# Kernel tuning notes

Hardware: AMD Instinct MI355X
Metric: run time of the kernel (lower is better)

Reference implementation:

```python
import jax, jax.numpy as jnp
import numpy as np

D = 1024
H = 16
HD = D // H  # 64

def setup_inputs() -> dict:
    key = jax.random.key(0)
    ks = jax.random.split(key, 7)
    B, S = 2, 2048
    x = jax.random.normal(ks[0], (B, S, D), dtype=jnp.float32)
    M = jax.random.randint(ks[1], (B, S, S), 0, 2, dtype=jnp.int32)
    s = 1.0 / np.sqrt(D)
    W_q = jax.random.normal(ks[2], (D, D), dtype=jnp.float32) * s
    W_k = jax.random.normal(ks[3], (D, D), dtype=jnp.float32) * s
    W_v = jax.random.normal(ks[4], (D, D), dtype=jnp.float32) * s
    W_o = jax.random.normal(ks[5], (D, D), dtype=jnp.float32) * s
    b_o = jax.random.normal(ks[6], (D,), dtype=jnp.float32) * 0.01
    return {"x": x, "M": M, "W_q": W_q, "W_k": W_k, "W_v": W_v, "W_o": W_o, "b_o": b_o}

def reference(x, M, W_q, W_k, W_v, W_o, b_o):
    B, S, _ = x.shape
    scale = HD ** -0.5
    # project and split heads: [B, H, S, HD]
    def heads(W):
        return (x @ W.T).reshape(B, S, H, HD).transpose(0, 2, 1, 3)
    Q, K, V = heads(W_q), heads(W_k), heads(W_v)
    scores = jnp.einsum('bhqd,bhkd->bhqk', Q, K) * scale
    mask = (M[:, None, :, :] == 0)  # broadcast over heads
    scores = jnp.where(mask, jnp.float32(-1e9), scores)
    A = jax.nn.softmax(scores, axis=-1)
    out = jnp.einsum('bhqk,bhkd->bhqd', A, V)
    out = out.transpose(0, 2, 1, 3).reshape(B, S, D)
    return out @ W_o.T + b_o
```

## Files before the change

### kernel.cpp

```cpp
#include <hip/hip_runtime.h>
#include <hip/hip_bf16.h>

typedef unsigned short u16;
typedef unsigned int u32;
typedef unsigned long long u64;
typedef _Float16 f16;
typedef __attribute__((__ext_vector_type__(4))) _Float16 f16x4;
typedef __attribute__((__ext_vector_type__(8))) short bf16x8;
typedef __attribute__((__ext_vector_type__(4))) float f32x4;
typedef __attribute__((__ext_vector_type__(16))) float f32x16;

__device__ __forceinline__ u16 f2bf(float f) {
    u32 u = __float_as_uint(f);
    return (u16)((u + 0x7fffu + ((u >> 16) & 1u)) >> 16);
}

__device__ __forceinline__ u32 pk2(float e, float o) {
    return (__float_as_uint(e) >> 16) | (__float_as_uint(o) & 0xFFFF0000u);
}

__global__ __launch_bounds__(256) void prep_kernel(
    const float4* __restrict__ x,  const float4* __restrict__ wq,
    const float4* __restrict__ wk, const float4* __restrict__ wv,
    const float4* __restrict__ wo,
    u16* __restrict__ xb, u16* __restrict__ wqb, u16* __restrict__ wkb,
    u16* __restrict__ wvb, u16* __restrict__ wob,
    const int* __restrict__ M, u64* __restrict__ Mb2)
{
    if (blockIdx.x < 8192) {
        int gid = blockIdx.x * 256 + threadIdx.x;
        const float4* src; u16* dst; int off;
        if (gid < 1048576) { src = x; dst = xb; off = gid; }
        else {
            int g = gid - 1048576;
            int sel = g >> 18;
            off = g & 262143;
            src = sel == 0 ? wq : sel == 1 ? wk : sel == 2 ? wv : wo;
            dst = sel == 0 ? wqb : sel == 1 ? wkb : sel == 2 ? wvb : wob;
        }
        float4 f = src[off];
        ushort4 o;
        o.x = f2bf(f.x); o.y = f2bf(f.y); o.z = f2bf(f.z); o.w = f2bf(f.w);
        ((ushort4*)dst)[off] = o;
    } else {
        int wg   = (blockIdx.x - 8192) * 4 + (threadIdx.x >> 6);
        int lane = threadIdx.x & 63;
        int w = wg & 31;
        int q = (wg >> 5) & 2047;
        int b = wg >> 16;
        size_t base = ((size_t)(b * 2048 + q)) * 2048 + w * 64 + lane;
        u64 bits = __ballot(M[base] != 0);
        if (lane == 0) Mb2[(size_t)(b * 32 + w) * 2048 + q] = bits;
    }
}

template<int MODE, int BN>
__global__ __launch_bounds__(256) void gemm_k(
    const u16* __restrict__ Ag, const u16* __restrict__ Bg,
    u16* __restrict__ Cq, u16* __restrict__ Kfr, u16* __restrict__ Vfr,
    float* __restrict__ Cf, const float* __restrict__ bias)
{
    constexpr int Kd = 1024;
    constexpr int NB = BN / 32;
    __shared__ u16 SM[8192 + BN * 64];
    u16* As0 = SM;
    u16* As1 = SM + 4096;
    u16* Bs0 = SM + 8192;
    u16* Bs1 = SM + 8192 + BN * 32;
    const int tid  = threadIdx.x;
    const int wave = tid >> 6, lane = tid & 63;
    const int quad = lane >> 4, l16 = lane & 15;
    const int n0 = blockIdx.x * BN;
    const int m0 = blockIdx.y * 128;

    const int wm = (wave & 1) * 64, wn = (wave >> 1) * (BN / 2);
    f32x4 acc[4][NB];
    #pragma unroll
    for (int i = 0; i < 4; i++)
        #pragma unroll
        for (int j = 0; j < NB; j++)
            acc[i][j] = (f32x4){0.f, 0.f, 0.f, 0.f};

    const int sr = lane >> 2;
    const int sk = (lane & 3) * 8;
    const int ca0 = wave * 2, ca1 = ca0 + 1;
    const u16* gA0 = Ag + (size_t)(m0 + ca0 * 16 + sr) * Kd + sk;
    const u16* gA1 = Ag + (size_t)(m0 + ca1 * 16 + sr) * Kd + sk;
    const int cb0 = (BN == 128) ? wave * 2 : wave;
    const u16* gB0 = Bg + (size_t)(n0 + cb0 * 16 + sr) * Kd + sk;
    const u16* gB1 = (BN == 128) ? Bg + (size_t)(n0 + (cb0 + 1) * 16 + sr) * Kd + sk : nullptr;

    #define GLL16(gp, lp) __builtin_amdgcn_global_load_lds( \
        (const __attribute__((address_space(1))) void*)(gp), \
        (__attribute__((address_space(3))) void*)(lp), 16, 0, 0)

    for (int k0 = 0; k0 < Kd; k0 += 64) {
        __syncthreads();
        GLL16(gA0 + k0, As0 + ca0 * 512);
        GLL16(gA1 + k0, As0 + ca1 * 512);
        GLL16(gB0 + k0, Bs0 + cb0 * 512);
        if (BN == 128) GLL16(gB1 + k0, Bs0 + (cb0 + 1) * 512);
        GLL16(gA0 + k0 + 32, As1 + ca0 * 512);
        GLL16(gA1 + k0 + 32, As1 + ca1 * 512);
        GLL16(gB0 + k0 + 32, Bs1 + cb0 * 512);
        if (BN == 128) GLL16(gB1 + k0 + 32, Bs1 + (cb0 + 1) * 512);
        __syncthreads();

        #pragma unroll
        for (int kk = 0; kk < 2; kk++) {
            const u16* Ah = kk ? As1 : As0;
            const u16* Bh = kk ? Bs1 : Bs0;
            bf16x8 af[4], bfr[NB];
            #pragma unroll
            for (int mb = 0; mb < 4; mb++)
                af[mb] = *(const bf16x8*)&Ah[(wm + mb * 16 + l16) * 32 + quad * 8];
            #pragma unroll
            for (int nb = 0; nb < NB; nb++)
                bfr[nb] = *(const bf16x8*)&Bh[(wn + nb * 16 + l16) * 32 + quad * 8];
            #pragma unroll
            for (int mb = 0; mb < 4; mb++)
                #pragma unroll
                for (int nb = 0; nb < NB; nb++)
                    acc[mb][nb] = __builtin_amdgcn_mfma_f32_16x16x32_bf16(
                        af[mb], bfr[nb], acc[mb][nb], 0, 0, 0);
        }
    }
    #undef GLL16

    if (MODE == 1) {
        #pragma unroll
        for (int mb = 0; mb < 4; mb++)
            #pragma unroll
            for (int nb = 0; nb < NB; nb++) {
                const int row = m0 + wm + mb * 16 + quad * 4;
                const int col = n0 + wn + nb * 16 + l16;
                #pragma unroll
                for (int r = 0; r < 4; r++)
                    Cf[(size_t)(row + r) * 1024 + col] = acc[mb][nb][r] + bias[col];
            }
        return;
    }

    const int region = n0 >> 10;
    if (region == 0) {
        #pragma unroll
        for (int mb = 0; mb < 4; mb++)
            #pragma unroll
            for (int nb = 0; nb < NB; nb++) {
                const int row = m0 + wm + mb * 16 + quad * 4;
                const int ccol = (n0 & 1023) + wn + nb * 16 + l16;
                #pragma unroll
                for (int r = 0; r < 4; r++)
                    Cq[(size_t)(row + r) * 1024 + ccol] =
                        f2bf(acc[mb][nb][r] * 0.18033688011112042f);
            }
        return;
    }

    const int bb = m0 >> 11;
    const int kt_base = (m0 & 2047) >> 6;
    const int head_base = (n0 & 1023) >> 6;
    u16* dst = (region == 1) ? Kfr : Vfr;
    #pragma unroll
    for (int pass = 0; pass < 2; pass++) {
        __syncthreads();
        #pragma unroll
        for (int mb = 0; mb < 4; mb++) {
            const int rowb = wm + mb * 16 + quad * 4;
            if ((rowb >> 6) != pass) continue;
            #pragma unroll
            for (int nb = 0; nb < NB; nb++) {
                const int ccol = wn + nb * 16 + l16;
                const int h2 = ccol >> 6, dd = ccol & 63;
                if (region == 1) {
                    const int t = dd >> 4, hik = (dd >> 3) & 1, j = dd & 7;
                    #pragma unroll
                    for (int r = 0; r < 4; r++) {
                        const int km = (rowb + r) & 63;
                        const int f = (km >> 5) * 4 + t;
                        const int lanek = hik * 32 + (km & 31);
                        SM[((h2 * 8 + f) * 64 + lanek) * 8 + j] = f2bf(acc[mb][nb][r]);
                    }
                } else {
                    const int kinb = rowb & 63;
                    const int t = kinb >> 4, hiv = (kinb >> 3) & 1, jb = kinb & 7;
                    const int f = (dd >> 5) * 4 + t;
                    const int lanev = hiv * 32 + (dd & 31);
                    ushort4 pk;
                    pk.x = f2bf(acc[mb][nb][0]); pk.y = f2bf(acc[mb][nb][1]);
                    pk.z = f2bf(acc[mb][nb][2]); pk.w = f2bf(acc[mb][nb][3]);
                    *(ushort4*)&SM[((h2 * 8 + f) * 64 + lanev) * 8 + jb] = pk;
                }
            }
        }
        __syncthreads();
        const int h2g = tid >> 7;
        const int inner = (tid & 127) * 32;
        const size_t gbase =
            ((size_t)(bb * 16 + head_base + h2g) * 32 + kt_base + pass) * 4096;
        #pragma unroll
        for (int c = 0; c < 4; c++)
            *(bf16x8*)&dst[gbase + inner + c * 8] =
                *(const bf16x8*)&SM[h2g * 4096 + inner + c * 8];
    }
}

__global__ __launch_bounds__(256) void attn_kernel(
    const u16* __restrict__ Qg, const u16* __restrict__ Kfr, const u16* __restrict__ Vfr,
    const u64* __restrict__ Mb2, f16* __restrict__ Opart, float* __restrict__ Lpart)
{
    const int qt = blockIdx.x >> 2;
    const int kh = blockIdx.x & 3;
    const int h  = blockIdx.y;
    const int b  = blockIdx.z;
    const int tid = threadIdx.x, wave = tid >> 6, lane = tid & 63;
    const int l31 = lane & 31, hi = lane >> 5;

    const int qrow0 = qt * 128 + wave * 32;
    const int bh    = b * 16 + h;

    bf16x8 qf[4];
    {
        const u16* qp = Qg + ((size_t)b * 2048 + qrow0 + l31) * 1024 + h * 64 + hi * 8;
        #pragma unroll
        for (int t = 0; t < 4; t++) qf[t] = *(const bf16x8*)(qp + t * 16);
    }

    const u16* kfp = Kfr + (size_t)bh * 131072 + lane * 8;
    const u16* vfp = Vfr + (size_t)bh * 131072 + lane * 8;

    f32x16 oacc0, oacc1;
    #pragma unroll
    for (int i = 0; i < 16; i++) { oacc0[i] = 0.f; oacc1[i] = 0.f; }
    float lsum = 0.f;

    const int kt0 = kh * 8;
    #pragma unroll 1
    for (int kt = kt0; kt < kt0 + 8; kt++) {
        const u64 mwv = Mb2[(size_t)(b * 32 + kt) * 2048 + qrow0 + l31];
        const u32 mlo = ((u32)mwv) >> (hi * 4);
        const u32 mhi = ((u32)(mwv >> 32)) >> (hi * 4);
        const size_t fb = (size_t)(kt * 8) * 512;

        #pragma unroll
        for (int ph = 0; ph < 2; ph++) {
            bf16x8 kf[4], vf[4];
            #pragma unroll
            for (int t = 0; t < 4; t++)
                kf[t] = *(const bf16x8*)(kfp + fb + (size_t)(ph * 4 + t) * 512);
            vf[0] = *(const bf16x8*)(vfp + fb + (size_t)(2 * ph) * 512);
            vf[1] = *(const bf16x8*)(vfp + fb + (size_t)(2 * ph + 1) * 512);
            vf[2] = *(const bf16x8*)(vfp + fb + (size_t)(4 + 2 * ph) * 512);
            vf[3] = *(const bf16x8*)(vfp + fb + (size_t)(4 + 2 * ph + 1) * 512);

            f32x16 s;
            #pragma unroll
            for (int i = 0; i < 16; i++) s[i] = 0.f;
            #pragma unroll
            for (int t = 0; t < 4; t++)
                s = __builtin_amdgcn_mfma_f32_32x32x16_bf16(kf[t], qf[t], s, 0, 0, 0);

            const u32 mm = ph ? mhi : mlo;
            #pragma unroll
            for (int reg = 0; reg < 16; reg++) {
                const int kb2 = (reg & 3) + 8 * (reg >> 2);
                float a = __builtin_amdgcn_exp2f(s[reg]);
                a = ((mm >> kb2) & 1u) ? a : 0.0f;
                s[reg] = a; lsum += a;
            }

            bf16x8 pb[2];
            #pragma unroll
            for (int fl = 0; fl < 2; fl++) {
                const int rb = 8 * fl;
                u32 a0 = pk2(s[rb], s[rb + 1]),     a1 = pk2(s[rb + 2], s[rb + 3]);
                u32 a2 = pk2(s[rb + 4], s[rb + 5]), a3 = pk2(s[rb + 6], s[rb + 7]);
                const u32 r0 = __shfl_xor(a0, 32);
                const u32 r1 = __shfl_xor(a1, 32);
                const u32 r2 = __shfl_xor(a2, 32);
                const u32 r3 = __shfl_xor(a3, 32);
                union { u32 u[4]; bf16x8 v; } fu;
                fu.u[0] = hi ? r2 : a0;
                fu.u[1] = hi ? r3 : a1;
                fu.u[2] = hi ? a2 : r0;
                fu.u[3] = hi ? a3 : r1;
                pb[fl] = fu.v;
            }

            oacc0 = __builtin_amdgcn_mfma_f32_32x32x16_bf16(vf[0], pb[0], oacc0, 0, 0, 0);
            oacc0 = __builtin_amdgcn_mfma_f32_32x32x16_bf16(vf[1], pb[1], oacc0, 0, 0, 0);
            oacc1 = __builtin_amdgcn_mfma_f32_32x32x16_bf16(vf[2], pb[0], oacc1, 0, 0, 0);
            oacc1 = __builtin_amdgcn_mfma_f32_32x32x16_bf16(vf[3], pb[1], oacc1, 0, 0, 0);
        }
    }

    lsum += __shfl_xor(lsum, 32);

    const size_t obase = ((size_t)(kh * 32 + bh) * 2048 + qrow0 + l31) * 64;
    #pragma unroll
    for (int tile = 0; tile < 2; tile++) {
        #pragma unroll
        for (int g = 0; g < 4; g++) {
            const int d0 = tile * 32 + g * 8 + hi * 4;
            f16x4 pkv;
            #pragma unroll
            for (int r = 0; r < 4; r++) {
                const int reg = g * 4 + r;
                pkv[r] = (f16)(tile == 0 ? oacc0[reg] : oacc1[reg]);
            }
            *(f16x4*)&Opart[obase + d0] = pkv;
        }
    }
    Lpart[(size_t)kh * 65536 + bh * 2048 + qrow0 + l31] = lsum;
}

__global__ __launch_bounds__(256) void merge_kernel(
    const f16* __restrict__ Opart, const float* __restrict__ Lpart,
    u16* __restrict__ AO)
{
    const int gid = blockIdx.x * 256 + threadIdx.x;
    const int c4 = gid & 15;
    const int q  = (gid >> 4) & 2047;
    const int bh = gid >> 15;
    const int b  = bh >> 4, h = bh & 15;

    float l = 0.f;
    float s0 = 0.f, s1 = 0.f, s2 = 0.f, s3 = 0.f;
    #pragma unroll
    for (int k = 0; k < 4; k++) {
        const size_t pbase = ((size_t)(k * 32 + bh) * 2048 + q) * 64 + c4 * 4;
        f16x4 o = *(const f16x4*)&Opart[pbase];
        s0 += (float)o[0]; s1 += (float)o[1]; s2 += (float)o[2]; s3 += (float)o[3];
        l += Lpart[(size_t)k * 65536 + bh * 2048 + q];
    }
    const float inv = 1.0f / l;
    ushort4 o;
    o.x = f2bf(s0 * inv); o.y = f2bf(s1 * inv);
    o.z = f2bf(s2 * inv); o.w = f2bf(s3 * inv);
    *(ushort4*)&AO[((size_t)b * 2048 + q) * 1024 + h * 64 + c4 * 4] = o;
}

extern "C" void kernel_launch(void* const* d_in, const int* in_sizes, int n_in,
                              void* d_out, int out_size, void* d_ws, size_t ws_size,
                              hipStream_t stream)
{
    const float* x  = (const float*)d_in[0];
    const int*   Mm = (const int*)d_in[1];
    const float* Wq = (const float*)d_in[2];
    const float* Wk = (const float*)d_in[3];
    const float* Wv = (const float*)d_in[4];
    const float* Wo = (const float*)d_in[5];
    const float* bo = (const float*)d_in[6];
    float* out = (float*)d_out;

    u16* ws  = (u16*)d_ws;
    u16* xb  = ws;
    u16* wqb = xb  + 4194304;
    u16* wkb = wqb + 1048576;
    u16* wvb = wkb + 1048576;
    u16* wob = wvb + 1048576;
    u16* Qb  = wob + 1048576;
    u16* Kfr = Qb  + 4194304;
    u16* Vfr = Kfr + 4194304;
    u16* AOb = Vfr + 4194304;
    u64* Mb2 = (u64*)(AOb + 4194304);
    f16* Opart = (f16*)(Mb2 + 131072);
    float* Lpart = (float*)(Opart + 16777216);

    prep_kernel<<<40960, 256, 0, stream>>>(
        (const float4*)x, (const float4*)Wq, (const float4*)Wk,
        (const float4*)Wv, (const float4*)Wo, xb, wqb, wkb, wvb, wob,
        Mm, Mb2);

    dim3 g1(24, 32, 1);
    gemm_k<0, 128><<<g1, 256, 0, stream>>>(xb, wqb, Qb, Kfr, Vfr, nullptr, nullptr);

    dim3 g2(64, 16, 2);
    attn_kernel<<<g2, 256, 0, stream>>>(Qb, Kfr, Vfr, Mb2, Opart, Lpart);

    merge_kernel<<<4096, 256, 0, stream>>>(Opart, Lpart, AOb);

    dim3 g3(16, 32, 1);
    gemm_k<1, 64><<<g3, 256, 0, stream>>>(AOb, wob, nullptr, nullptr, nullptr,
                                          out, bo);
}
```

Measured before the change: 237.7 us.

## Fold mask into MFMA init, compute row sums via MFMA, use permlane32 swap

```diff
diff --git a/kernel.cpp b/kernel.cpp
--- a/kernel.cpp
+++ b/kernel.cpp
@@ -9,14 +9,11 @@
 typedef __attribute__((__ext_vector_type__(8))) short bf16x8;
 typedef __attribute__((__ext_vector_type__(4))) float f32x4;
 typedef __attribute__((__ext_vector_type__(16))) float f32x16;
+typedef __attribute__((__ext_vector_type__(2))) int i32x2;
 
 __device__ __forceinline__ u16 f2bf(float f) {
     u32 u = __float_as_uint(f);
     return (u16)((u + 0x7fffu + ((u >> 16) & 1u)) >> 16);
-}
-
-__device__ __forceinline__ u32 pk2(float e, float o) {
-    return (__float_as_uint(e) >> 16) | (__float_as_uint(o) & 0xFFFF0000u);
 }
 
 __global__ __launch_bounds__(256) void prep_kernel(
@@ -226,13 +223,15 @@
         for (int t = 0; t < 4; t++) qf[t] = *(const bf16x8*)(qp + t * 16);
     }
 
-    const u16* kfp = Kfr + (size_t)bh * 131072 + lane * 8;
-    const u16* vfp = Vfr + (size_t)bh * 131072 + lane * 8;
-
-    f32x16 oacc0, oacc1;
-    #pragma unroll
-    for (int i = 0; i < 16; i++) { oacc0[i] = 0.f; oacc1[i] = 0.f; }
-    float lsum = 0.f;
+    const u32 fro = (u32)bh * 131072u + (u32)lane * 8u;
+
+    bf16x8 ones;
+    #pragma unroll
+    for (int j = 0; j < 8; j++) ones[j] = (short)0x3F80;
+
+    f32x16 oacc0, oacc1, lacc;
+    #pragma unroll
+    for (int i = 0; i < 16; i++) { oacc0[i] = 0.f; oacc1[i] = 0.f; lacc[i] = 0.f; }
 
     const int kt0 = kh * 8;
     #pragma unroll 1
@@ -240,50 +239,52 @@
         const u64 mwv = Mb2[(size_t)(b * 32 + kt) * 2048 + qrow0 + l31];
         const u32 mlo = ((u32)mwv) >> (hi * 4);
         const u32 mhi = ((u32)(mwv >> 32)) >> (hi * 4);
-        const size_t fb = (size_t)(kt * 8) * 512;
+        const u32 fb = fro + (u32)kt * 4096u;
 
         #pragma unroll
         for (int ph = 0; ph < 2; ph++) {
             bf16x8 kf[4], vf[4];
             #pragma unroll
             for (int t = 0; t < 4; t++)
-                kf[t] = *(const bf16x8*)(kfp + fb + (size_t)(ph * 4 + t) * 512);
-            vf[0] = *(const bf16x8*)(vfp + fb + (size_t)(2 * ph) * 512);
-            vf[1] = *(const bf16x8*)(vfp + fb + (size_t)(2 * ph + 1) * 512);
-            vf[2] = *(const bf16x8*)(vfp + fb + (size_t)(4 + 2 * ph) * 512);
-            vf[3] = *(const bf16x8*)(vfp + fb + (size_t)(4 + 2 * ph + 1) * 512);
-
+                kf[t] = *(const bf16x8*)(Kfr + fb + (u32)(ph * 4 + t) * 512u);
+            vf[0] = *(const bf16x8*)(Vfr + fb + (u32)(2 * ph) * 512u);
+            vf[1] = *(const bf16x8*)(Vfr + fb + (u32)(2 * ph + 1) * 512u);
+            vf[2] = *(const bf16x8*)(Vfr + fb + (u32)(4 + 2 * ph) * 512u);
+            vf[3] = *(const bf16x8*)(Vfr + fb + (u32)(4 + 2 * ph + 1) * 512u);
+
+            const u32 mn = ~(ph ? mhi : mlo);
             f32x16 s;
             #pragma unroll
-            for (int i = 0; i < 16; i++) s[i] = 0.f;
+            for (int reg = 0; reg < 16; reg++) {
+                const int kb2 = (reg & 3) + 8 * (reg >> 2);
+                s[reg] = __int_as_float(
+                    __builtin_amdgcn_sbfe((int)mn, kb2, 1) & (int)0xFF800000);
+            }
             #pragma unroll
             for (int t = 0; t < 4; t++)
                 s = __builtin_amdgcn_mfma_f32_32x32x16_bf16(kf[t], qf[t], s, 0, 0, 0);
 
-            const u32 mm = ph ? mhi : mlo;
-            #pragma unroll
-            for (int reg = 0; reg < 16; reg++) {
-                const int kb2 = (reg & 3) + 8 * (reg >> 2);
-                float a = __builtin_amdgcn_exp2f(s[reg]);
-                a = ((mm >> kb2) & 1u) ? a : 0.0f;
-                s[reg] = a; lsum += a;
+            u32 w[8];
+            #pragma unroll
+            for (int i = 0; i < 8; i++) {
+                const float e0 = __builtin_amdgcn_exp2f(s[2 * i]);
+                const float e1 = __builtin_amdgcn_exp2f(s[2 * i + 1]);
+                w[i] = __builtin_amdgcn_perm(__float_as_uint(e1),
+                                             __float_as_uint(e0), 0x07060302u);
             }
 
             bf16x8 pb[2];
             #pragma unroll
             for (int fl = 0; fl < 2; fl++) {
-                const int rb = 8 * fl;
-                u32 a0 = pk2(s[rb], s[rb + 1]),     a1 = pk2(s[rb + 2], s[rb + 3]);
-                u32 a2 = pk2(s[rb + 4], s[rb + 5]), a3 = pk2(s[rb + 6], s[rb + 7]);
-                const u32 r0 = __shfl_xor(a0, 32);
-                const u32 r1 = __shfl_xor(a1, 32);
-                const u32 r2 = __shfl_xor(a2, 32);
-                const u32 r3 = __shfl_xor(a3, 32);
+                i32x2 p02 = __builtin_amdgcn_permlane32_swap(
+                    (int)w[4 * fl + 0], (int)w[4 * fl + 2], false, false);
+                i32x2 p13 = __builtin_amdgcn_permlane32_swap(
+                    (int)w[4 * fl + 1], (int)w[4 * fl + 3], false, false);
                 union { u32 u[4]; bf16x8 v; } fu;
-                fu.u[0] = hi ? r2 : a0;
-                fu.u[1] = hi ? r3 : a1;
-                fu.u[2] = hi ? a2 : r0;
-                fu.u[3] = hi ? a3 : r1;
+                fu.u[0] = (u32)p02[0];
+                fu.u[1] = (u32)p13[0];
+                fu.u[2] = (u32)p02[1];
+                fu.u[3] = (u32)p13[1];
                 pb[fl] = fu.v;
             }
 
@@ -291,10 +292,10 @@
             oacc0 = __builtin_amdgcn_mfma_f32_32x32x16_bf16(vf[1], pb[1], oacc0, 0, 0, 0);
             oacc1 = __builtin_amdgcn_mfma_f32_32x32x16_bf16(vf[2], pb[0], oacc1, 0, 0, 0);
             oacc1 = __builtin_amdgcn_mfma_f32_32x32x16_bf16(vf[3], pb[1], oacc1, 0, 0, 0);
-        }
-    }
-
-    lsum += __shfl_xor(lsum, 32);
+            lacc  = __builtin_amdgcn_mfma_f32_32x32x16_bf16(ones,  pb[0], lacc,  0, 0, 0);
+            lacc  = __builtin_amdgcn_mfma_f32_32x32x16_bf16(ones,  pb[1], lacc,  0, 0, 0);
+        }
+    }
 
     const size_t obase = ((size_t)(kh * 32 + bh) * 2048 + qrow0 + l31) * 64;
     #pragma unroll
@@ -311,7 +312,7 @@
             *(f16x4*)&Opart[obase + d0] = pkv;
         }
     }
-    Lpart[(size_t)kh * 65536 + bh * 2048 + qrow0 + l31] = lsum;
+    Lpart[(size_t)kh * 65536 + bh * 2048 + qrow0 + l31] = lacc[0];
 }
 
 __global__ __launch_bounds__(256) void merge_kernel(
```

New measurement: 239.9 us. About the same (+0.9%).
